# Performance work log

Hardware: AMD Instinct MI355X
Metric: run time of the kernel (lower is better)

Reference implementation:

```python
import jax, jax.numpy as jnp
import numpy as np

HORIZON_K = 20
EPS = 1e-8


def _unfold_gather(x, time_idx, k):
    # Emulates zero-pad + tensor.unfold(1, k, 1).permute(3,0,1,2) + index_select(2, time_idx)
    # x: [N, T-1, C] -> [k, N, S, C] where out[ki, n, s] = x_padded[n, time_idx[s] + ki]
    N, Tm1, C = x.shape
    xp = jnp.concatenate([x, jnp.zeros((N, k, C), x.dtype)], axis=1)
    gidx = time_idx[None, :] + jnp.arange(k)[:, None]  # [k, S]
    return jnp.transpose(xp[:, gidx, :], (1, 0, 2, 3))  # [k, N, S, C]


def _gru_rollout(x_seq, h0, W_ih, W_hh, b_ih, b_hh):
    # x_seq: [k, B, A]; h0: [B, H]; torch GRU gate order: r, z, n
    H = h0.shape[-1]
    def step(h, x):
        gi = x @ W_ih.T + b_ih          # [B, 3H]
        gh = h @ W_hh.T + b_hh          # [B, 3H]
        r = jax.nn.sigmoid(gi[:, :H] + gh[:, :H])
        z = jax.nn.sigmoid(gi[:, H:2 * H] + gh[:, H:2 * H])
        n = jnp.tanh(gi[:, 2 * H:] + r * gh[:, 2 * H:])
        hn = (1.0 - z) * n + z * h
        return hn, hn
    _, hs = jax.lax.scan(step, h0, x_seq)
    return hs  # [k, B, H]


def _mlp(x, W1, b1, W2, b2, W3, b3):
    x = jax.nn.relu(x @ W1 + b1)
    x = jax.nn.relu(x @ W2 + b2)
    return x @ W3 + b3


def _l2norm(x):
    n = jnp.linalg.norm(x, axis=-1, keepdims=True)
    return x / jnp.maximum(n, EPS)


def setup_inputs() -> dict:
    key = jax.random.key(0)
    ks = jax.random.split(key, 16)
    N, T, H, A, M = 1024, 128, 256, 18, 512
    g = lambda k, sh, s: jax.random.normal(k, sh, jnp.float32) * s
    return {
        "actions": jax.random.randint(ks[0], (N, T), 0, A),
        "dones": jnp.zeros((N, T), jnp.float32),
        "b_t": g(ks[1], (N * T, H), 1.0),
        "z_t": g(ks[2], (N * T, H), 1.0),
        "time_subsample": jax.random.randint(ks[3], (6,), 0, T - 1),
        "unroll_subsample": jax.random.randint(ks[4], (2,), 0, HORIZON_K),
        "W_ih": g(ks[5], (3 * H, A), 0.05), "W_hh": g(ks[6], (3 * H, H), 0.05),
        "b_ih": g(ks[7], (3 * H,), 0.05), "b_hh": g(ks[8], (3 * H,), 0.05),
        "W1": g(ks[9], (H, M), 0.05), "b1": g(ks[10], (M,), 0.05),
        "W2": g(ks[11], (M, M), 0.05), "b2": g(ks[12], (M,), 0.05),
        "W3": g(ks[13], (M, H), 0.05), "b3": g(ks[14], (H,), 0.05),
    }


def reference(actions, dones, b_t, z_t, time_subsample, unroll_subsample,
              W_ih, W_hh, b_ih, b_hh, W1, b1, W2, b2, W3, b3):
    N, T = actions.shape
    H = b_t.shape[-1]
    A = W_ih.shape[1]
    k = HORIZON_K

    # mask (dones fixed to all-zero -> max_k == horizon_k)
    not_dones = (1.0 - dones).reshape(N, T, 1)
    nd_unf = _unfold_gather(not_dones[:, :-1], time_subsample, k)        # [k,N,S,1]
    fmask = jnp.cumprod(nd_unf, axis=0).reshape(k, -1, 1)                # [k,N*S,1]
    fmask = (fmask[unroll_subsample] > 0).astype(jnp.float32)            # [F,B,1]

    # unfolded one-hot actions
    onehot = jax.nn.one_hot(actions, A, dtype=jnp.float32)               # [N,T,A]
    act_unf = _unfold_gather(onehot[:, :-1], time_subsample, k)          # [k,N,S,A]
    act_unf = act_unf.reshape(k, -1, A)                                  # [k,B,A]

    # GRU initial states from core outputs at subsampled times
    c = b_t.reshape(N, T, H)[:, :-1][:, time_subsample]                  # [N,S,H]
    h0 = c.reshape(-1, H)                                                # [B,H]

    # 20-step open-loop GRU rollout
    h_pred = _gru_rollout(act_unf, h0, W_ih, W_hh, b_ih, b_hh)           # [k,B,H]
    h_pred = h_pred[unroll_subsample]                                    # [F,B,H]

    final_pred = _mlp(h_pred, W1, b1, W2, b2, W3, b3)                    # [F,B,H]
    norm = jnp.linalg.norm(final_pred, axis=2)
    reg = 0.02 * jnp.square(norm - 1.0)                                  # [F,B]
    final_pred = _l2norm(final_pred)

    # targets (no grad): unfolded future encodings, normalized
    z = jax.lax.stop_gradient(z_t).reshape(N, T, -1)
    tgt = _unfold_gather(z[:, 1:], time_subsample, k)                    # [k,N,S,C]
    tgt = tgt[unroll_subsample].reshape(len(unroll_subsample), -1, z.shape[-1])
    tgt = _l2norm(tgt)                                                   # [F,B,C]

    loss = jnp.square(final_pred - tgt)                                  # [F,B,C]
    loss = loss.mean(-1, keepdims=True)                                  # [F,B,1]
    loss = jnp.sum(loss * fmask) / jnp.maximum(jnp.sum(fmask), 1.0)
    return loss + reg.mean()
```

## Files before the change

kernel.cpp:

```cpp
#include <hip/hip_runtime.h>
#include <hip/hip_bf16.h>
#include <math.h>

#define NN 1024
#define TT 128
#define SS 6
#define FF 2
#define HH 256
#define AA 18
#define MM 512
#define KH 20
#define BB (NN*SS)
#define RR (FF*BB)

#define SCL_RZ (-1.44269504089f)
#define SCL_N  (-2.88539008178f)
#define TBLP_STRIDE 129

typedef __bf16 bf16x8 __attribute__((ext_vector_type(8)));
typedef float f32x4 __attribute__((ext_vector_type(4)));

__device__ __forceinline__ f32x4 mfma16(bf16x8 a, bf16x8 b, f32x4 c) {
    return __builtin_amdgcn_mfma_f32_16x16x32_bf16(a, b, c, 0, 0, 0);
}
__device__ __forceinline__ unsigned short f2b(float f) {
    return __builtin_bit_cast(unsigned short, __float2bfloat16(f));
}
__device__ __forceinline__ float b2f(unsigned short u) {
    return __builtin_bit_cast(float, (unsigned)u << 16);
}
__device__ __forceinline__ float blo(unsigned u) {
    return __builtin_bit_cast(float, u << 16);
}
__device__ __forceinline__ float bhi(unsigned u) {
    return __builtin_bit_cast(float, u & 0xffff0000u);
}
__device__ __forceinline__ float rcp_f(float x)  { return __builtin_amdgcn_rcpf(x); }
__device__ __forceinline__ float exp2_f(float x) { return __builtin_amdgcn_exp2f(x); }

#define OFF_ACT   0UL
#define OFF_HPRED 491520UL
#define OFF_WHH   6782976UL
#define OFF_W1T   7176192UL
#define OFF_W2T   7438336UL
#define OFF_W3T   7962624UL
#define OFF_TBL   8224768UL
#define OFF_PART  8264000UL

__global__ void k_prep(const float* __restrict__ Whh, const float* __restrict__ W1,
                       const float* __restrict__ W2, const float* __restrict__ W3,
                       const float* __restrict__ Wih, const float* __restrict__ bih,
                       const float* __restrict__ bhh,
                       const int* __restrict__ actions, const int* __restrict__ ts,
                       unsigned short* whh_s, unsigned short* w1t, unsigned short* w2t,
                       unsigned short* w3t, uint4* tblp, int* act) {
    int idx = blockIdx.x * 256 + threadIdx.x;
    if (idx < 196608) {
        int wrow = idx >> 8;
        float scl = (wrow < 512) ? SCL_RZ : SCL_N;
        whh_s[idx] = f2b(Whh[idx] * scl);
        return;
    }
    idx -= 196608;
    if (idx < 131072) { int m = idx >> 8, k = idx & 255; w1t[idx] = f2b(W1[k * MM + m]); return; }
    idx -= 131072;
    if (idx < 262144) { int m = idx >> 9, k = idx & 511; w2t[idx] = f2b(W2[k * MM + m]); return; }
    idx -= 262144;
    if (idx < 131072) { int c = idx >> 9, k = idx & 511; w3t[idx] = f2b(W3[k * HH + c]); return; }
    idx -= 131072;
    if (idx < 19 * TBLP_STRIDE) {
        int a = idx / TBLP_STRIDE, jp = idx - a * TBLP_STRIDE;
        uint4 o = {0u, 0u, 0u, 0u};
        if (jp < 128) {
            int j0 = jp * 2, j1 = j0 + 1;
            float wr0 = (a < AA) ? Wih[j0 * AA + a] : 0.f;
            float wr1 = (a < AA) ? Wih[j1 * AA + a] : 0.f;
            float wz0 = (a < AA) ? Wih[(256 + j0) * AA + a] : 0.f;
            float wz1 = (a < AA) ? Wih[(256 + j1) * AA + a] : 0.f;
            float wn0 = (a < AA) ? Wih[(512 + j0) * AA + a] : 0.f;
            float wn1 = (a < AA) ? Wih[(512 + j1) * AA + a] : 0.f;
            float r0 = SCL_RZ * (wr0 + bih[j0] + bhh[j0]);
            float r1 = SCL_RZ * (wr1 + bih[j1] + bhh[j1]);
            float z0 = SCL_RZ * (wz0 + bih[256 + j0] + bhh[256 + j0]);
            float z1 = SCL_RZ * (wz1 + bih[256 + j1] + bhh[256 + j1]);
            float n0 = SCL_N * (wn0 + bih[512 + j0]);
            float n1 = SCL_N * (wn1 + bih[512 + j1]);
            o.x = (unsigned)f2b(r0) | ((unsigned)f2b(r1) << 16);
            o.y = (unsigned)f2b(z0) | ((unsigned)f2b(z1) << 16);
            o.z = (unsigned)f2b(n0) | ((unsigned)f2b(n1) << 16);
        }
        tblp[idx] = o;
        return;
    }
    idx -= 19 * TBLP_STRIDE;
    if (idx < BB * KH) {
        int b = idx / KH, k = idx - b * KH;
        int n = b / SS, s = b - n * SS;
        int tt = ts[s] + k;
        act[idx] = (tt < TT - 1) ? actions[n * TT + tt] : AA;
    }
}

__global__ void __launch_bounds__(512, 2)
k_gru_all(const unsigned short* __restrict__ whh_s, const uint4* __restrict__ tblpg,
          const float* __restrict__ bhh, const int* __restrict__ actg,
          const int* __restrict__ us, const int* __restrict__ ts,
          const float* __restrict__ b_t, unsigned short* __restrict__ hpred) {
    __shared__ uint4 tbl[19 * TBLP_STRIDE];
    __shared__ alignas(16) unsigned short htile[2][32][264];
    __shared__ int act_l[32][KH];

    int tid = threadIdx.x, wave = tid >> 6, lane = tid & 63;
    int l15 = lane & 15, grp = lane >> 4, lk8 = grp << 3, r4 = grp << 2;
    int rb = blockIdx.x * 24;
    int u0 = us[0], u1 = us[1];
    int kmax = u0 > u1 ? u0 : u1;
    int j0 = wave * 32 + 2 * l15;
    int jp = wave * 16 + l15;

    for (int i = tid; i < 19 * TBLP_STRIDE; i += 512) tbl[i] = tblpg[i];
    if (tid < 32 * KH) {
        int r = tid / KH, k2 = tid - r * KH;
        act_l[r][k2] = (r < 24) ? actg[(rb + r) * KH + k2] : AA;
    }

    bf16x8 wr[6][8];
#pragma unroll
    for (int ct = 0; ct < 6; ++ct) {
        int wrow = (ct >> 1) * 256 + j0 + (ct & 1);
        const unsigned short* base = &whh_s[(size_t)wrow * HH];
#pragma unroll
        for (int kk = 0; kk < 8; ++kk)
            wr[ct][kk] = *reinterpret_cast<const bf16x8*>(&base[kk * 32 + lk8]);
    }
    float bhn0 = SCL_N * bhh[512 + j0];
    float bhn1 = SCL_N * bhh[512 + j0 + 1];

    unsigned hmp[2][4];
#pragma unroll
    for (int rt = 0; rt < 2; ++rt)
#pragma unroll
        for (int reg = 0; reg < 4; ++reg) {
            int rowl = rt * 16 + r4 + reg;
            unsigned hv = 0u;
            if (rowl < 24) {
                int b = rb + rowl;
                int n = b / SS, s = b - n * SS;
                const float* src = &b_t[(size_t)(n * TT + ts[s]) * HH + j0];
                hv = (unsigned)f2b(src[0]) | ((unsigned)f2b(src[1]) << 16);
            }
            hmp[rt][reg] = hv;
        }

    for (int i = tid; i < 2 * 32 * 32; i += 512) {
        int buf = i >> 10, rem = i & 1023, row = rem >> 5, c8 = (rem & 31) << 3;
        uint4 pk = {0u, 0u, 0u, 0u};
        if (buf == 0 && row < 24) {
            int b = rb + row;
            int n = b / SS, s = b - n * SS;
            const float* src = &b_t[(size_t)(n * TT + ts[s]) * HH + c8];
            pk.x = f2b(src[0]) | ((unsigned)f2b(src[1]) << 16);
            pk.y = f2b(src[2]) | ((unsigned)f2b(src[3]) << 16);
            pk.z = f2b(src[4]) | ((unsigned)f2b(src[5]) << 16);
            pk.w = f2b(src[6]) | ((unsigned)f2b(src[7]) << 16);
        }
        *reinterpret_cast<uint4*>(&htile[buf][row][c8]) = pk;
    }
    __syncthreads();

    int cur = 0;
    for (int ki = 0; ki <= kmax; ++ki) {
        int nxt = cur ^ 1;
#pragma unroll
        for (int rt = 0; rt < 2; ++rt) {
            f32x4 aR[2] = {}, aZ[2] = {}, aN[2] = {};
#pragma unroll
            for (int kk = 0; kk < 8; ++kk) {
                bf16x8 ah = *reinterpret_cast<const bf16x8*>(&htile[cur][rt * 16 + l15][kk * 32 + lk8]);
                aR[0] = mfma16(ah, wr[0][kk], aR[0]);
                aR[1] = mfma16(ah, wr[1][kk], aR[1]);
                aZ[0] = mfma16(ah, wr[2][kk], aZ[0]);
                aZ[1] = mfma16(ah, wr[3][kk], aZ[1]);
                aN[0] = mfma16(ah, wr[4][kk], aN[0]);
                aN[1] = mfma16(ah, wr[5][kk], aN[1]);
            }
#pragma unroll
            for (int reg = 0; reg < 4; ++reg) {
                int rowl = rt * 16 + r4 + reg;
                uint4 gi = tbl[act_l[rowl][ki] * TBLP_STRIDE + jp];
                float r0 = rcp_f(1.f + exp2_f(aR[0][reg] + blo(gi.x)));
                float r1 = rcp_f(1.f + exp2_f(aR[1][reg] + bhi(gi.x)));
                float z0 = rcp_f(1.f + exp2_f(aZ[0][reg] + blo(gi.y)));
                float z1 = rcp_f(1.f + exp2_f(aZ[1][reg] + bhi(gi.y)));
                float tv0 = blo(gi.z) + r0 * (aN[0][reg] + bhn0);
                float tv1 = bhi(gi.z) + r1 * (aN[1][reg] + bhn1);
                float nv0 = 2.f * rcp_f(1.f + exp2_f(tv0)) - 1.f;
                float nv1 = 2.f * rcp_f(1.f + exp2_f(tv1)) - 1.f;
                unsigned hp = hmp[rt][reg];
                float hn0 = nv0 + z0 * (blo(hp) - nv0);
                float hn1 = nv1 + z1 * (bhi(hp) - nv1);
                unsigned hv = (unsigned)f2b(hn0) | ((unsigned)f2b(hn1) << 16);
                hmp[rt][reg] = hv;
                if (rowl < 24) {
                    *reinterpret_cast<unsigned*>(&htile[nxt][rowl][j0]) = hv;
                    if (ki == u0)
                        *reinterpret_cast<unsigned*>(&hpred[(size_t)(rb + rowl) * HH + j0]) = hv;
                    if (ki == u1)
                        *reinterpret_cast<unsigned*>(&hpred[(size_t)(BB + rb + rowl) * HH + j0]) = hv;
                }
            }
        }
        __syncthreads();
        cur = nxt;
    }
}

__device__ __forceinline__ int xsw(int row, int chunk) {
    return (row << 9) + ((chunk ^ (row & 7)) << 3);
}

__global__ void __launch_bounds__(512, 4)
k_mlp_loss(const unsigned short* __restrict__ hpred, const unsigned short* __restrict__ w1t,
           const unsigned short* __restrict__ w2t, const unsigned short* __restrict__ w3t,
           const float* __restrict__ b1, const float* __restrict__ b2,
           const float* __restrict__ b3, const float* __restrict__ z_t,
           const float* __restrict__ dones, const int* __restrict__ ts,
           const int* __restrict__ us, float* __restrict__ part) {
    __shared__ unsigned short xs[48 * 512];
    __shared__ unsigned short zs[48 * 256];
    __shared__ float rstat[48][8][3];
    __shared__ float vmask[48];

    int tid = threadIdx.x, wave = tid >> 6, lane = tid & 63;
    int l15 = lane & 15, grp = lane >> 4, lk8 = grp << 3, r4 = grp << 2;
    int rb = blockIdx.x * 48;

    if (tid < 48) {
        int rg = rb + tid;
        int f = rg >= BB ? 1 : 0;
        int b = rg - f * BB;
        int n = b / SS, s = b - n * SS;
        int t = ts[s], u = us[f];
        float m = (t + u < TT - 1) ? 1.f : 0.f;
        if (m > 0.f) for (int jj = 0; jj <= u; ++jj) m *= (1.f - dones[n * TT + t + jj]);
        vmask[tid] = (m > 0.f) ? 1.f : 0.f;
    }
    for (int i = tid; i < 48 * 64; i += 512) {
        int row = i >> 6, c4 = (i & 63) << 2;
        int rg = rb + row;
        int f = rg >= BB ? 1 : 0;
        int b = rg - f * BB;
        int n = b / SS, s = b - n * SS;
        int t = ts[s], u = us[f];
        uint2 pk = {0u, 0u};
        if (t + u < TT - 1) {
            float4 v = *reinterpret_cast<const float4*>(&z_t[(size_t)(n * TT + 1 + t + u) * HH + c4]);
            pk.x = f2b(v.x) | ((unsigned)f2b(v.y) << 16);
            pk.y = f2b(v.z) | ((unsigned)f2b(v.w) << 16);
        }
        *reinterpret_cast<uint2*>(&zs[row * 256 + c4]) = pk;
    }

    {
        f32x4 acc[3][4] = {};
        for (int kk = 0; kk < 8; ++kk) {
            int k0 = kk * 32 + lk8;
            bf16x8 av[3];
#pragma unroll
            for (int rt = 0; rt < 3; ++rt)
                av[rt] = *reinterpret_cast<const bf16x8*>(&hpred[(size_t)(rb + rt * 16 + l15) * HH + k0]);
#pragma unroll
            for (int ct = 0; ct < 4; ++ct) {
                int col = wave * 64 + ct * 16 + l15;
                bf16x8 bv = *reinterpret_cast<const bf16x8*>(&w1t[(size_t)col * HH + k0]);
#pragma unroll
                for (int rt = 0; rt < 3; ++rt) acc[rt][ct] = mfma16(av[rt], bv, acc[rt][ct]);
            }
        }
#pragma unroll
        for (int ct = 0; ct < 4; ++ct) {
            int col = wave * 64 + ct * 16 + l15;
            float bb = b1[col];
#pragma unroll
            for (int rt = 0; rt < 3; ++rt)
#pragma unroll
                for (int reg = 0; reg < 4; ++reg)
                    xs[xsw(rt * 16 + r4 + reg, col >> 3) + (col & 7)] =
                        f2b(fmaxf(acc[rt][ct][reg] + bb, 0.f));
        }
    }
    __syncthreads();

    {
        f32x4 acc[3][4] = {};
        for (int kk = 0; kk < 16; ++kk) {
            bf16x8 av[3];
#pragma unroll
            for (int rt = 0; rt < 3; ++rt)
                av[rt] = *reinterpret_cast<const bf16x8*>(&xs[xsw(rt * 16 + l15, kk * 4 + grp)]);
#pragma unroll
            for (int ct = 0; ct < 4; ++ct) {
                int col = wave * 64 + ct * 16 + l15;
                bf16x8 bv = *reinterpret_cast<const bf16x8*>(&w2t[(size_t)col * MM + kk * 32 + lk8]);
#pragma unroll
                for (int rt = 0; rt < 3; ++rt) acc[rt][ct] = mfma16(av[rt], bv, acc[rt][ct]);
            }
        }
        __syncthreads();
#pragma unroll
        for (int ct = 0; ct < 4; ++ct) {
            int col = wave * 64 + ct * 16 + l15;
            float bb = b2[col];
#pragma unroll
            for (int rt = 0; rt < 3; ++rt)
#pragma unroll
                for (int reg = 0; reg < 4; ++reg)
                    xs[xsw(rt * 16 + r4 + reg, col >> 3) + (col & 7)] =
                        f2b(fmaxf(acc[rt][ct][reg] + bb, 0.f));
        }
    }
    __syncthreads();

    {
        f32x4 acc[3][2] = {};
        for (int kk = 0; kk < 16; ++kk) {
            bf16x8 av[3];
#pragma unroll
            for (int rt = 0; rt < 3; ++rt)
                av[rt] = *reinterpret_cast<const bf16x8*>(&xs[xsw(rt * 16 + l15, kk * 4 + grp)]);
#pragma unroll
            for (int ct = 0; ct < 2; ++ct) {
                int col = wave * 32 + ct * 16 + l15;
                bf16x8 bv = *reinterpret_cast<const bf16x8*>(&w3t[(size_t)col * MM + kk * 32 + lk8]);
#pragma unroll
                for (int rt = 0; rt < 3; ++rt) acc[rt][ct] = mfma16(av[rt], bv, acc[rt][ct]);
            }
        }
        float b3c0 = b3[wave * 32 + l15];
        float b3c1 = b3[wave * 32 + 16 + l15];
#pragma unroll
        for (int rt = 0; rt < 3; ++rt)
#pragma unroll
            for (int reg = 0; reg < 4; ++reg) {
                int row = rt * 16 + r4 + reg;
                float p0 = acc[rt][0][reg] + b3c0;
                float p1 = acc[rt][1][reg] + b3c1;
                float z0 = b2f(zs[row * 256 + wave * 32 + l15]);
                float z1 = b2f(zs[row * 256 + wave * 32 + 16 + l15]);
                float psq = p0 * p0 + p1 * p1;
                float zsq = z0 * z0 + z1 * z1;
                float pz  = p0 * z0 + p1 * z1;
#pragma unroll
                for (int o = 1; o < 16; o <<= 1) {
                    psq += __shfl_xor(psq, o);
                    zsq += __shfl_xor(zsq, o);
                    pz  += __shfl_xor(pz, o);
                }
                if (l15 == 0) {
                    rstat[row][wave][0] = psq;
                    rstat[row][wave][1] = zsq;
                    rstat[row][wave][2] = pz;
                }
            }
    }
    __syncthreads();

    if (tid < 64) {
        float a0 = 0.f, a1 = 0.f, a2 = 0.f;
        if (tid < 48) {
            float sp = 0.f, sz = 0.f, spz = 0.f;
#pragma unroll
            for (int w = 0; w < 8; ++w) {
                sp  += rstat[tid][w][0];
                sz  += rstat[tid][w][1];
                spz += rstat[tid][w][2];
            }
            float npn = sqrtf(sp), nzn = sqrtf(sz);
            float d = npn - 1.f;
            a2 = 0.02f * d * d;
            float mp = fmaxf(npn, 1e-8f), mz = fmaxf(nzn, 1e-8f);
            float lossr = (sp / (mp * mp) + sz / (mz * mz) - 2.f * spz / (mp * mz)) * (1.f / HH);
            float vm = vmask[tid];
            a0 = vm * lossr;
            a1 = vm;
        }
#pragma unroll
        for (int o = 1; o < 64; o <<= 1) {
            a0 += __shfl_xor(a0, o);
            a1 += __shfl_xor(a1, o);
            a2 += __shfl_xor(a2, o);
        }
        if (tid == 0) {
            part[blockIdx.x * 3 + 0] = a0;
            part[blockIdx.x * 3 + 1] = a1;
            part[blockIdx.x * 3 + 2] = a2;
        }
    }
}

__global__ void k_final(const float* __restrict__ part, float* out) {
    int tid = threadIdx.x, wave = tid >> 6, lane = tid & 63;
    float s0 = part[tid * 3 + 0];
    float s1 = part[tid * 3 + 1];
    float s2 = part[tid * 3 + 2];
    for (int o = 32; o; o >>= 1) {
        s0 += __shfl_xor(s0, o);
        s1 += __shfl_xor(s1, o);
        s2 += __shfl_xor(s2, o);
    }
    __shared__ float sm[4][3];
    if (lane == 0) { sm[wave][0] = s0; sm[wave][1] = s1; sm[wave][2] = s2; }
    __syncthreads();
    if (tid == 0) {
        float a = 0.f, b = 0.f, c = 0.f;
        for (int w = 0; w < 4; ++w) { a += sm[w][0]; b += sm[w][1]; c += sm[w][2]; }
        out[0] = a / fmaxf(b, 1.f) + c * (1.f / RR);
    }
}

extern "C" void kernel_launch(void* const* d_in, const int* in_sizes, int n_in,
                              void* d_out, int out_size, void* d_ws, size_t ws_size,
                              hipStream_t stream) {
    const int*   actions = (const int*)d_in[0];
    const float* dones   = (const float*)d_in[1];
    const float* b_t     = (const float*)d_in[2];
    const float* z_t     = (const float*)d_in[3];
    const int*   ts      = (const int*)d_in[4];
    const int*   us      = (const int*)d_in[5];
    const float* W_ih    = (const float*)d_in[6];
    const float* W_hh    = (const float*)d_in[7];
    const float* b_ih    = (const float*)d_in[8];
    const float* b_hh    = (const float*)d_in[9];
    const float* W1      = (const float*)d_in[10];
    const float* b1      = (const float*)d_in[11];
    const float* W2      = (const float*)d_in[12];
    const float* b2      = (const float*)d_in[13];
    const float* W3      = (const float*)d_in[14];
    const float* b3      = (const float*)d_in[15];

    char* ws = (char*)d_ws;
    int*            act   = (int*)(ws + OFF_ACT);
    unsigned short* hpred = (unsigned short*)(ws + OFF_HPRED);
    unsigned short* whh_s = (unsigned short*)(ws + OFF_WHH);
    unsigned short* w1t   = (unsigned short*)(ws + OFF_W1T);
    unsigned short* w2t   = (unsigned short*)(ws + OFF_W2T);
    unsigned short* w3t   = (unsigned short*)(ws + OFF_W3T);
    uint4*          tblp  = (uint4*)(ws + OFF_TBL);
    float*          part  = (float*)(ws + OFF_PART);

    k_prep<<<3306, 256, 0, stream>>>(W_hh, W1, W2, W3, W_ih, b_ih, b_hh, actions, ts,
                                     whh_s, w1t, w2t, w3t, tblp, act);
    k_gru_all<<<256, 512, 0, stream>>>(whh_s, tblp, b_hh, act, us, ts, b_t, hpred);
    k_mlp_loss<<<256, 512, 0, stream>>>(hpred, w1t, w2t, w3t, b1, b2, b3,
                                        z_t, dones, ts, us, part);
    k_final<<<1, 256, 0, stream>>>(part, (float*)d_out);
}
```

Baseline: 116.4 us.

## Fuse GRU rollout, MLP loss and final reduction into one kernel

Merges the GRU rollout and the MLP/loss kernels so that each block keeps its predicted hidden states in shared memory instead of writing them to global memory and reading them back. The row mapping is changed so one block handles both unroll snapshots for its 24 batch rows. The separate final-reduction kernel is replaced by a last-block-done atomic counter that sums the partials. Two kernel launches and a global round trip are removed, but the fused kernel runs under the GRU's launch bounds of 2 blocks per CU rather than 4 for the MLP part. It also uses about 100 KB of aliased shared memory.

```diff
diff --git a/kernel.cpp b/kernel.cpp
--- a/kernel.cpp
+++ b/kernel.cpp
@@ -29,23 +29,28 @@
 __device__ __forceinline__ float b2f(unsigned short u) {
     return __builtin_bit_cast(float, (unsigned)u << 16);
 }
-__device__ __forceinline__ float blo(unsigned u) {
-    return __builtin_bit_cast(float, u << 16);
-}
-__device__ __forceinline__ float bhi(unsigned u) {
-    return __builtin_bit_cast(float, u & 0xffff0000u);
-}
+__device__ __forceinline__ float blo(unsigned u) { return __builtin_bit_cast(float, u << 16); }
+__device__ __forceinline__ float bhi(unsigned u) { return __builtin_bit_cast(float, u & 0xffff0000u); }
 __device__ __forceinline__ float rcp_f(float x)  { return __builtin_amdgcn_rcpf(x); }
 __device__ __forceinline__ float exp2_f(float x) { return __builtin_amdgcn_exp2f(x); }
 
 #define OFF_ACT   0UL
-#define OFF_HPRED 491520UL
-#define OFF_WHH   6782976UL
-#define OFF_W1T   7176192UL
-#define OFF_W2T   7438336UL
-#define OFF_W3T   7962624UL
-#define OFF_TBL   8224768UL
-#define OFF_PART  8264000UL
+#define OFF_WHH   491520UL
+#define OFF_W1T   884736UL
+#define OFF_W2T   1146880UL
+#define OFF_W3T   1671168UL
+#define OFF_TBL   1933312UL
+#define OFF_PART  1972528UL
+#define OFF_CNT   1975600UL
+
+#define SM_HTILE 39216
+#define SM_ACT   73008
+#define SM_XS    0
+#define SM_ZS    49152
+#define SM_RSTAT 73728
+#define SM_VMASK 78336
+#define SM_SNAP  78528
+#define SM_TOTAL 103872
 
 __global__ void k_prep(const float* __restrict__ Whh, const float* __restrict__ W1,
                        const float* __restrict__ W2, const float* __restrict__ W3,
@@ -53,7 +58,8 @@
                        const float* __restrict__ bhh,
                        const int* __restrict__ actions, const int* __restrict__ ts,
                        unsigned short* whh_s, unsigned short* w1t, unsigned short* w2t,
-                       unsigned short* w3t, uint4* tblp, int* act) {
+                       unsigned short* w3t, uint4* tblp, int* act, unsigned* cnt) {
+    if (blockIdx.x == 0 && threadIdx.x == 0) *cnt = 0u;
     int idx = blockIdx.x * 256 + threadIdx.x;
     if (idx < 196608) {
         int wrow = idx >> 8;
@@ -101,14 +107,30 @@
     }
 }
 
+__device__ __forceinline__ int xsw(int row, int chunk) {
+    return (row << 9) + ((chunk ^ (row & 7)) << 3);
+}
+
 __global__ void __launch_bounds__(512, 2)
-k_gru_all(const unsigned short* __restrict__ whh_s, const uint4* __restrict__ tblpg,
-          const float* __restrict__ bhh, const int* __restrict__ actg,
-          const int* __restrict__ us, const int* __restrict__ ts,
-          const float* __restrict__ b_t, unsigned short* __restrict__ hpred) {
-    __shared__ uint4 tbl[19 * TBLP_STRIDE];
-    __shared__ alignas(16) unsigned short htile[2][32][264];
-    __shared__ int act_l[32][KH];
+k_fused(const unsigned short* __restrict__ whh_s, const uint4* __restrict__ tblpg,
+        const float* __restrict__ bhh, const int* __restrict__ actg,
+        const int* __restrict__ us, const int* __restrict__ ts,
+        const float* __restrict__ b_t,
+        const unsigned short* __restrict__ w1t, const unsigned short* __restrict__ w2t,
+        const unsigned short* __restrict__ w3t, const float* __restrict__ b1,
+        const float* __restrict__ b2, const float* __restrict__ b3,
+        const float* __restrict__ z_t, const float* __restrict__ dones,
+        float* __restrict__ part, unsigned* __restrict__ cnt, float* __restrict__ out) {
+    __shared__ alignas(16) char smem[SM_TOTAL];
+    __shared__ unsigned ord;
+    uint4* tbl = (uint4*)smem;
+    unsigned short (*htile)[32][264] = (unsigned short (*)[32][264])(smem + SM_HTILE);
+    int (*act_l)[KH] = (int (*)[KH])(smem + SM_ACT);
+    unsigned short* xs = (unsigned short*)(smem + SM_XS);
+    unsigned short* zs = (unsigned short*)(smem + SM_ZS);
+    float (*rstat)[8][3] = (float (*)[8][3])(smem + SM_RSTAT);
+    float* vmask = (float*)(smem + SM_VMASK);
+    unsigned short* snap = (unsigned short*)(smem + SM_SNAP);
 
     int tid = threadIdx.x, wave = tid >> 6, lane = tid & 63;
     int l15 = lane & 15, grp = lane >> 4, lk8 = grp << 3, r4 = grp << 2;
@@ -119,8 +141,8 @@
     int jp = wave * 16 + l15;
 
     for (int i = tid; i < 19 * TBLP_STRIDE; i += 512) tbl[i] = tblpg[i];
-    if (tid < 32 * KH) {
-        int r = tid / KH, k2 = tid - r * KH;
+    for (int i = tid; i < 32 * KH; i += 512) {
+        int r = i / KH, k2 = i - r * KH;
         act_l[r][k2] = (r < 24) ? actg[(rb + r) * KH + k2] : AA;
     }
 
@@ -204,41 +226,19 @@
                 if (rowl < 24) {
                     *reinterpret_cast<unsigned*>(&htile[nxt][rowl][j0]) = hv;
                     if (ki == u0)
-                        *reinterpret_cast<unsigned*>(&hpred[(size_t)(rb + rowl) * HH + j0]) = hv;
+                        *reinterpret_cast<unsigned*>(&snap[rowl * 264 + j0]) = hv;
                     if (ki == u1)
-                        *reinterpret_cast<unsigned*>(&hpred[(size_t)(BB + rb + rowl) * HH + j0]) = hv;
+                        *reinterpret_cast<unsigned*>(&snap[(24 + rowl) * 264 + j0]) = hv;
                 }
             }
         }
         __syncthreads();
         cur = nxt;
     }
-}
-
-__device__ __forceinline__ int xsw(int row, int chunk) {
-    return (row << 9) + ((chunk ^ (row & 7)) << 3);
-}
-
-__global__ void __launch_bounds__(512, 4)
-k_mlp_loss(const unsigned short* __restrict__ hpred, const unsigned short* __restrict__ w1t,
-           const unsigned short* __restrict__ w2t, const unsigned short* __restrict__ w3t,
-           const float* __restrict__ b1, const float* __restrict__ b2,
-           const float* __restrict__ b3, const float* __restrict__ z_t,
-           const float* __restrict__ dones, const int* __restrict__ ts,
-           const int* __restrict__ us, float* __restrict__ part) {
-    __shared__ unsigned short xs[48 * 512];
-    __shared__ unsigned short zs[48 * 256];
-    __shared__ float rstat[48][8][3];
-    __shared__ float vmask[48];
-
-    int tid = threadIdx.x, wave = tid >> 6, lane = tid & 63;
-    int l15 = lane & 15, grp = lane >> 4, lk8 = grp << 3, r4 = grp << 2;
-    int rb = blockIdx.x * 48;
 
     if (tid < 48) {
-        int rg = rb + tid;
-        int f = rg >= BB ? 1 : 0;
-        int b = rg - f * BB;
+        int f = tid / 24, lr = tid - f * 24;
+        int b = rb + lr;
         int n = b / SS, s = b - n * SS;
         int t = ts[s], u = us[f];
         float m = (t + u < TT - 1) ? 1.f : 0.f;
@@ -247,9 +247,8 @@
     }
     for (int i = tid; i < 48 * 64; i += 512) {
         int row = i >> 6, c4 = (i & 63) << 2;
-        int rg = rb + row;
-        int f = rg >= BB ? 1 : 0;
-        int b = rg - f * BB;
+        int f = row / 24, lr = row - f * 24;
+        int b = rb + lr;
         int n = b / SS, s = b - n * SS;
         int t = ts[s], u = us[f];
         uint2 pk = {0u, 0u};
@@ -268,7 +267,7 @@
             bf16x8 av[3];
 #pragma unroll
             for (int rt = 0; rt < 3; ++rt)
-                av[rt] = *reinterpret_cast<const bf16x8*>(&hpred[(size_t)(rb + rt * 16 + l15) * HH + k0]);
+                av[rt] = *reinterpret_cast<const bf16x8*>(&snap[(rt * 16 + l15) * 264 + k0]);
 #pragma unroll
             for (int ct = 0; ct < 4; ++ct) {
                 int col = wave * 64 + ct * 16 + l15;
@@ -394,27 +393,27 @@
             part[blockIdx.x * 3 + 0] = a0;
             part[blockIdx.x * 3 + 1] = a1;
             part[blockIdx.x * 3 + 2] = a2;
-        }
-    }
-}
-
-__global__ void k_final(const float* __restrict__ part, float* out) {
-    int tid = threadIdx.x, wave = tid >> 6, lane = tid & 63;
-    float s0 = part[tid * 3 + 0];
-    float s1 = part[tid * 3 + 1];
-    float s2 = part[tid * 3 + 2];
-    for (int o = 32; o; o >>= 1) {
-        s0 += __shfl_xor(s0, o);
-        s1 += __shfl_xor(s1, o);
-        s2 += __shfl_xor(s2, o);
-    }
-    __shared__ float sm[4][3];
-    if (lane == 0) { sm[wave][0] = s0; sm[wave][1] = s1; sm[wave][2] = s2; }
+            __threadfence();
+            ord = atomicAdd(cnt, 1u);
+        }
+    }
     __syncthreads();
-    if (tid == 0) {
-        float a = 0.f, b = 0.f, c = 0.f;
-        for (int w = 0; w < 4; ++w) { a += sm[w][0]; b += sm[w][1]; c += sm[w][2]; }
-        out[0] = a / fmaxf(b, 1.f) + c * (1.f / RR);
+
+    if (ord == 255u && tid < 64) {
+        __threadfence();
+        float s0 = 0.f, s1 = 0.f, s2 = 0.f;
+        for (int i = tid; i < 256; i += 64) {
+            s0 += part[i * 3 + 0];
+            s1 += part[i * 3 + 1];
+            s2 += part[i * 3 + 2];
+        }
+#pragma unroll
+        for (int o = 1; o < 64; o <<= 1) {
+            s0 += __shfl_xor(s0, o);
+            s1 += __shfl_xor(s1, o);
+            s2 += __shfl_xor(s2, o);
+        }
+        if (tid == 0) out[0] = s0 / fmaxf(s1, 1.f) + s2 * (1.f / RR);
     }
 }
 
@@ -440,18 +439,17 @@
 
     char* ws = (char*)d_ws;
     int*            act   = (int*)(ws + OFF_ACT);
-    unsigned short* hpred = (unsigned short*)(ws + OFF_HPRED);
     unsigned short* whh_s = (unsigned short*)(ws + OFF_WHH);
     unsigned short* w1t   = (unsigned short*)(ws + OFF_W1T);
     unsigned short* w2t   = (unsigned short*)(ws + OFF_W2T);
     unsigned short* w3t   = (unsigned short*)(ws + OFF_W3T);
     uint4*          tblp  = (uint4*)(ws + OFF_TBL);
     float*          part  = (float*)(ws + OFF_PART);
+    unsigned*       cnt   = (unsigned*)(ws + OFF_CNT);
 
     k_prep<<<3306, 256, 0, stream>>>(W_hh, W1, W2, W3, W_ih, b_ih, b_hh, actions, ts,
-                                     whh_s, w1t, w2t, w3t, tblp, act);
-    k_gru_all<<<256, 512, 0, stream>>>(whh_s, tblp, b_hh, act, us, ts, b_t, hpred);
-    k_mlp_loss<<<256, 512, 0, stream>>>(hpred, w1t, w2t, w3t, b1, b2, b3,
-                                        z_t, dones, ts, us, part);
-    k_final<<<1, 256, 0, stream>>>(part, (float*)d_out);
-}
+                                     whh_s, w1t, w2t, w3t, tblp, act, cnt);
+    k_fused<<<256, 512, 0, stream>>>(whh_s, tblp, b_hh, act, us, ts, b_t,
+                                     w1t, w2t, w3t, b1, b2, b3, z_t, dones,
+                                     part, cnt, (float*)d_out);
+}
```

Measured after the change: 95.98 us. 1.21x faster.
